# Optimization experiments

Hardware: AMD Instinct MI355X
Metric: run time of the kernel (lower is better)

## Reference

```python
import jax, jax.numpy as jnp
import numpy as np

IN_DIM = 1024
OUT_DIM = 1024
NHEAD = 16
K = 9  # template(1032) - dim(1024) + 1


def _slinear(vec, template, conv_w, conv_b, lin_b):
    # Conv2d over template produces the [out_dim, in_dim] weight matrix.
    w = jax.lax.conv_general_dilated(
        template, conv_w, window_strides=(1, 1), padding='VALID',
        dimension_numbers=('NCHW', 'OIHW', 'NCHW'))  # [1,1,out_dim,in_dim]
    w = w[0, 0] + conv_b  # broadcast conv bias (scalar per out-channel)
    return vec @ w.T + lin_b  # F.linear(vec, w) + bias


def setup_inputs() -> dict:
    key = jax.random.key(0)
    ks = jax.random.split(key, 13)
    S, B = 2048, 2
    d = {
        'query': jax.random.normal(ks[0], (S, B, IN_DIM), jnp.float32),
        'key': jax.random.normal(ks[1], (S, B, IN_DIM), jnp.float32),
        'value': jax.random.normal(ks[2], (S, B, IN_DIM), jnp.float32),
        'template': jax.random.normal(ks[3], (1, 1, 1032, 1032), jnp.float32),
    }
    for i, name in enumerate(['wq', 'wk', 'wv']):
        d[name + '_cw'] = jax.random.normal(ks[4 + 3 * i], (1, 1, K, K), jnp.float32) * 0.05
        d[name + '_cb'] = jax.random.normal(ks[5 + 3 * i], (1,), jnp.float32) * 0.05
        d[name + '_b'] = jax.random.normal(ks[6 + 3 * i], (OUT_DIM,), jnp.float32) * 0.05
    return d


def reference(query, key, value, template,
              wq_cw, wq_cb, wq_b, wk_cw, wk_cb, wk_b, wv_cw, wv_cb, wv_b):
    q = _slinear(query, template, wq_cw, wq_cb, wq_b)
    k = _slinear(key, template, wk_cw, wk_cb, wk_b)
    v = _slinear(value, template, wv_cw, wv_cb, wv_b)
    S, B = q.shape[0], q.shape[1]
    h_dim = OUT_DIM // NHEAD
    scale = h_dim ** 0.5
    qh = q.reshape(S, B, NHEAD, h_dim)
    kh = k.reshape(S, B, NHEAD, h_dim)
    vh = v.reshape(S, B, NHEAD, h_dim)
    # batch_first=False path: scores then softmax over last dim
    scores = jnp.einsum('ibhd,jbhd->bhij', qh, kh) / scale  # [B,H,S,S]
    attn = jax.nn.softmax(scores, axis=-1)
    out = jnp.einsum('bhij,jbhd->ibhd', attn, vh).reshape(S, B, OUT_DIM)
    return out
```

## Files before the change

### kernel.cpp

```cpp
#include <hip/hip_runtime.h>
#include <math.h>

#define TDIM   1032
#define DIM    1024
#define SLEN   2048
#define BATCH  2
#define NROWS  (SLEN*BATCH)
#define NHEAD  16
#define HD     64

typedef unsigned short u16;
typedef short short8 __attribute__((ext_vector_type(8)));
typedef short bf16x4 __attribute__((ext_vector_type(4)));
typedef float f32x4  __attribute__((ext_vector_type(4)));

#define CSCALE 0.18033688011112042f

__device__ inline unsigned fbits(float x) {
    union { float f; unsigned u; } v; v.f = x; return v.u;
}
__device__ inline float asfloat(unsigned u) {
    union { unsigned u; float f; } v; v.u = u; return v.f;
}
__device__ inline u16 f2bf_rne(float x) {
    unsigned u = fbits(x);
    unsigned r = u + 0x7fffu + ((u >> 16) & 1u);
    return (u16)(r >> 16);
}
__device__ inline float bf2f(u16 b) { return asfloat(((unsigned)b) << 16); }
__device__ inline void dma16(const u16* g, u16* l) {
    __builtin_amdgcn_global_load_lds(
        (const __attribute__((address_space(1))) void*)g,
        (__attribute__((address_space(3))) void*)l, 16, 0, 0);
}

__global__ __launch_bounds__(256) void conv_weight_kernel(
    const float* __restrict__ tmpl,
    const float* __restrict__ cw0, const float* __restrict__ cb0,
    const float* __restrict__ cw1, const float* __restrict__ cb1,
    const float* __restrict__ cw2, const float* __restrict__ cb2,
    u16* __restrict__ Wh, u16* __restrict__ Wl)
{
    int t = blockIdx.z;
    const float* cw = (t == 0) ? cw0 : ((t == 1) ? cw1 : cw2);
    const float* cb = (t == 0) ? cb0 : ((t == 1) ? cb1 : cb2);
    __shared__ float scw[81];
    if (threadIdx.x < 81) scw[threadIdx.x] = cw[threadIdx.x];
    __syncthreads();
    int i = blockIdx.x * 256 + threadIdx.x;
    int o = blockIdx.y;
    float acc = cb[0];
    #pragma unroll
    for (int dy = 0; dy < 9; ++dy) {
        const float* trow = tmpl + (size_t)(o + dy) * TDIM + i;
        #pragma unroll
        for (int dx = 0; dx < 9; ++dx)
            acc = fmaf(scw[dy * 9 + dx], trow[dx], acc);
    }
    size_t idx = (size_t)t * DIM * DIM + (size_t)o * DIM + i;
    u16 h = f2bf_rne(acc);
    Wh[idx] = h;
    Wl[idx] = f2bf_rne(acc - bf2f(h));
}

__global__ __launch_bounds__(256, 3) void qkv_mfma_gemm(
    const float* __restrict__ x0, const float* __restrict__ x1,
    const float* __restrict__ x2,
    const u16* __restrict__ Whg, const u16* __restrict__ Wlg,
    const float* __restrict__ b0, const float* __restrict__ b1,
    const float* __restrict__ b2,
    u16* __restrict__ Qh, u16* __restrict__ Ql,
    u16* __restrict__ Kh, u16* __restrict__ Kl,
    u16* __restrict__ Vb)
{
    int t = blockIdx.z;
    const float* X    = (t == 0) ? x0 : ((t == 1) ? x1 : x2);
    const u16* Bh_g   = Whg + (size_t)t * DIM * DIM;
    const u16* Bl_g   = Wlg + (size_t)t * DIM * DIM;
    const float* bias = (t == 0) ? b0 : ((t == 1) ? b1 : b2);

    __shared__ __align__(16) u16 lds[16384];
    u16* sAh = lds;
    u16* sAl = lds + 4096;
    u16* sBh = lds + 8192;
    u16* sBl = lds + 12288;

    int tid = threadIdx.x;
    int w = tid >> 6, lane = tid & 63;
    int c = lane & 15, quad = lane >> 4;
    int m0 = blockIdx.y * 128, n0 = blockIdx.x * 128;
    int mh = (w >> 1) * 64, nh = (w & 1) * 64;

    int arow = w * 32 + (lane & 31);
    int acol = (lane >> 5) * 16;
    const float* aptr = X + (size_t)(m0 + arow) * DIM + acol;

    int srow = lane >> 2, sgr = lane & 3;

    f32x4 acc[4][4];
    #pragma unroll
    for (int i = 0; i < 4; ++i)
        #pragma unroll
        for (int j = 0; j < 4; ++j)
            #pragma unroll
            for (int r = 0; r < 4; ++r) acc[i][j][r] = 0.0f;

    float bias_v[4];
    #pragma unroll
    for (int tn = 0; tn < 4; ++tn) bias_v[tn] = bias[n0 + nh + tn * 16 + c];

    float4 xa[4];
    #pragma unroll
    for (int i = 0; i < 2; ++i) {
        int rb = w * 32 + i * 16;
        const u16* gh = Bh_g + (size_t)(n0 + rb + srow) * DIM + sgr * 8;
        const u16* gl = Bl_g + (size_t)(n0 + rb + srow) * DIM + sgr * 8;
        dma16(gh, sBh + rb * 32);
        dma16(gl, sBl + rb * 32);
    }
    #pragma unroll
    for (int j = 0; j < 4; ++j) xa[j] = *(const float4*)(aptr + j * 4);

    for (int it = 0; it < 32; ++it) {
        #pragma unroll
        for (int g = 0; g < 2; ++g) {
            float v[8] = { xa[2*g].x, xa[2*g].y, xa[2*g].z, xa[2*g].w,
                           xa[2*g+1].x, xa[2*g+1].y, xa[2*g+1].z, xa[2*g+1].w };
            short8 hv, lv;
            #pragma unroll
            for (int e = 0; e < 8; ++e) {
                unsigned u = fbits(v[e]);
                hv[e] = (short)(u >> 16);
                float l = v[e] - asfloat(u & 0xffff0000u);
                lv[e] = (short)(fbits(l) >> 16);
            }
            *(short8*)(sAh + arow * 32 + acol + g * 8) = hv;
            *(short8*)(sAl + arow * 32 + acol + g * 8) = lv;
        }
        __syncthreads();

        short8 ah[4], al[4], bh[4], bl[4];
        #pragma unroll
        for (int tt = 0; tt < 4; ++tt) {
            int mi = (mh + tt * 16 + c) * 32 + quad * 8;
            ah[tt] = *(short8*)(sAh + mi);
            al[tt] = *(short8*)(sAl + mi);
            int ni = (nh + tt * 16 + c) * 32 + quad * 8;
            bh[tt] = *(short8*)(sBh + ni);
            bl[tt] = *(short8*)(sBl + ni);
        }
        __syncthreads();

        if (it < 31) {
            int kg = (it + 1) * 4;
            #pragma unroll
            for (int i = 0; i < 2; ++i) {
                int rb = w * 32 + i * 16;
                const u16* gh = Bh_g + (size_t)(n0 + rb + srow) * DIM + (kg + sgr) * 8;
                const u16* gl = Bl_g + (size_t)(n0 + rb + srow) * DIM + (kg + sgr) * 8;
                dma16(gh, sBh + rb * 32);
                dma16(gl, sBl + rb * 32);
            }
            #pragma unroll
            for (int j = 0; j < 4; ++j)
                xa[j] = *(const float4*)(aptr + (it + 1) * 32 + j * 4);
        }

        #pragma unroll
        for (int tm = 0; tm < 4; ++tm)
            #pragma unroll
            for (int tn = 0; tn < 4; ++tn) {
                acc[tm][tn] = __builtin_amdgcn_mfma_f32_16x16x32_bf16(
                    ah[tm], bh[tn], acc[tm][tn], 0, 0, 0);
                acc[tm][tn] = __builtin_amdgcn_mfma_f32_16x16x32_bf16(
                    ah[tm], bl[tn], acc[tm][tn], 0, 0, 0);
                acc[tm][tn] = __builtin_amdgcn_mfma_f32_16x16x32_bf16(
                    al[tm], bh[tn], acc[tm][tn], 0, 0, 0);
            }
    }

    if (t < 2) {
        u16* Yh = (t == 0) ? Qh : Kh;
        u16* Yl = (t == 0) ? Ql : Kl;
        float qs = (t == 0) ? CSCALE : 1.0f;
        #pragma unroll
        for (int tm = 0; tm < 4; ++tm)
            #pragma unroll
            for (int r = 0; r < 4; ++r) {
                int m = m0 + mh + tm * 16 + quad * 4 + r;
                #pragma unroll
                for (int tn = 0; tn < 4; ++tn) {
                    int n = n0 + nh + tn * 16 + c;
                    float o = (acc[tm][tn][r] + bias_v[tn]) * qs;
                    unsigned bo = fbits(o);
                    Yh[(size_t)m * DIM + n] = (u16)(bo >> 16);
                    float l = o - asfloat(bo & 0xffff0000u);
                    Yl[(size_t)m * DIM + n] = (u16)(fbits(l) >> 16);
                }
            }
    } else {
        #pragma unroll
        for (int tm = 0; tm < 4; ++tm)
            #pragma unroll
            for (int r = 0; r < 4; ++r) {
                int m = m0 + mh + tm * 16 + quad * 4 + r;
                #pragma unroll
                for (int tn = 0; tn < 4; ++tn) {
                    int n = n0 + nh + tn * 16 + c;
                    Vb[(size_t)m * DIM + n] =
                        (u16)(fbits(acc[tm][tn][r] + bias_v[tn]) >> 16);
                }
            }
    }
}

__global__ __launch_bounds__(256) void vt_kernel(
    const u16* __restrict__ Vb, u16* __restrict__ Vt)
{
    int b = blockIdx.z, h = blockIdx.y, s0 = blockIdx.x * 64;
    __shared__ __align__(16) u16 tile[64][80];
    int tid = threadIdx.x;
    int sl = tid >> 2, d0 = (tid & 3) * 16;
    const u16* src = Vb + (size_t)((s0 + sl) * BATCH + b) * DIM + h * HD + d0;
    short8 v0 = *(const short8*)src;
    short8 v1 = *(const short8*)(src + 8);
    #pragma unroll
    for (int j = 0; j < 8; ++j) {
        tile[d0 + j][sl] = (u16)v0[j];
        tile[d0 + 8 + j][sl] = (u16)v1[j];
    }
    __syncthreads();
    int d = tid >> 2, sc0 = (tid & 3) * 16;
    u16* dst = Vt + (size_t)((b * NHEAD + h) * HD + d) * SLEN + s0 + sc0;
    *(short8*)dst = *(const short8*)&tile[d][sc0];
    *(short8*)(dst + 8) = *(const short8*)&tile[d][sc0 + 8];
}

__global__ __launch_bounds__(256) void attn_mfma_kernel(
    const u16* __restrict__ Qh, const u16* __restrict__ Ql,
    const u16* __restrict__ Kh, const u16* __restrict__ Kl,
    const u16* __restrict__ Vt, float* __restrict__ out)
{
    int b = blockIdx.z, h = blockIdx.y;
    int q0 = blockIdx.x * 128;
    int tid = threadIdx.x;
    int w = tid >> 6, lane = tid & 63;
    int c = lane & 15, quad = lane >> 4;

    __shared__ __align__(16) u16 sbuf[2][3][4096];
    __shared__ __align__(16) u16 sP[4][2048];

    short8 qhf[2][2], qlf[2][2];
    #pragma unroll
    for (int u = 0; u < 2; ++u) {
        int s = q0 + w * 32 + u * 16 + c;
        size_t base = (size_t)(s * BATCH + b) * DIM + h * HD + quad * 8;
        qhf[u][0] = *(const short8*)(Qh + base);
        qhf[u][1] = *(const short8*)(Qh + base + 32);
        qlf[u][0] = *(const short8*)(Ql + base);
        qlf[u][1] = *(const short8*)(Ql + base + 32);
    }

    f32x4 acc[2][4];
    #pragma unroll
    for (int u = 0; u < 2; ++u)
        #pragma unroll
        for (int i = 0; i < 4; ++i)
            #pragma unroll
            for (int r = 0; r < 4; ++r) acc[u][i][r] = 0.0f;
    float m_run[2] = {-1e38f, -1e38f}, l_run[2] = {0.0f, 0.0f};

    int r3 = lane >> 3, c3 = lane & 7;
    int sw = c3 ^ r3;
    const size_t bhofs = (size_t)(b * NHEAD + h) * HD;

    #define ISSUE_DMA(n0v, bufv) do {                                          \
        _Pragma("unroll")                                                      \
        for (int j = 0; j < 2; ++j) {                                          \
            int i_ = 2 * w + j;                                                \
            int row_ = i_ * 8 + r3;                                            \
            size_t gk = (size_t)(((n0v) + row_) * BATCH + b) * DIM + h * HD + sw * 8; \
            dma16(Kh + gk, &sbuf[bufv][0][i_ * 512]);                          \
            dma16(Kl + gk, &sbuf[bufv][1][i_ * 512]);                          \
            size_t gv = (bhofs + row_) * SLEN + (n0v) + sw * 8;                \
            dma16(Vt + gv, &sbuf[bufv][2][i_ * 512]);                          \
        }                                                                      \
    } while (0)

    ISSUE_DMA(0, 0);

    for (int it = 0; it < 32; ++it) {
        int cur = it & 1;
        __syncthreads();
        if (it < 31) ISSUE_DMA((it + 1) * 64, cur ^ 1);

        const u16* bKh = sbuf[cur][0];
        const u16* bKl = sbuf[cur][1];
        const u16* bVt = sbuf[cur][2];

        f32x4 sc[2][4];
        #pragma unroll
        for (int ct = 0; ct < 4; ++ct) {
            int row = ct * 16 + c, rw = row & 7;
            int kb = row * 64;
            short8 kh0 = *(const short8*)(bKh + kb + ((quad ^ rw) * 8));
            short8 kh1 = *(const short8*)(bKh + kb + (((4 + quad) ^ rw) * 8));
            short8 kl0 = *(const short8*)(bKl + kb + ((quad ^ rw) * 8));
            short8 kl1 = *(const short8*)(bKl + kb + (((4 + quad) ^ rw) * 8));
            #pragma unroll
            for (int u = 0; u < 2; ++u) {
                f32x4 s = {0.0f, 0.0f, 0.0f, 0.0f};
                s = __builtin_amdgcn_mfma_f32_16x16x32_bf16(kh0, qhf[u][0], s, 0, 0, 0);
                s = __builtin_amdgcn_mfma_f32_16x16x32_bf16(kh1, qhf[u][1], s, 0, 0, 0);
                s = __builtin_amdgcn_mfma_f32_16x16x32_bf16(kh0, qlf[u][0], s, 0, 0, 0);
                s = __builtin_amdgcn_mfma_f32_16x16x32_bf16(kh1, qlf[u][1], s, 0, 0, 0);
                s = __builtin_amdgcn_mfma_f32_16x16x32_bf16(kl0, qhf[u][0], s, 0, 0, 0);
                s = __builtin_amdgcn_mfma_f32_16x16x32_bf16(kl1, qhf[u][1], s, 0, 0, 0);
                sc[u][ct] = s;
            }
        }

        u16* wp = sP[w];
        #pragma unroll
        for (int u = 0; u < 2; ++u) {
            float pm = sc[u][0][0];
            #pragma unroll
            for (int ct = 0; ct < 4; ++ct)
                #pragma unroll
                for (int r = 0; r < 4; ++r)
                    pm = fmaxf(pm, sc[u][ct][r]);
            pm = fmaxf(pm, __shfl_xor(pm, 16));
            pm = fmaxf(pm, __shfl_xor(pm, 32));
            float mnew = fmaxf(m_run[u], pm);
            float al = exp2f(m_run[u] - mnew);
            m_run[u] = mnew;
            float ps = 0.0f;
            int prow = (u * 16 + c) * 64;
            #pragma unroll
            for (int ct = 0; ct < 4; ++ct) {
                bf16x4 pk;
                #pragma unroll
                for (int r = 0; r < 4; ++r) {
                    float p = exp2f(sc[u][ct][r] - mnew);
                    ps += p;
                    pk[r] = (short)(fbits(p) >> 16);
                }
                int phys = (ct * 2 + (quad >> 1)) ^ (c & 7);
                *(bf16x4*)(wp + prow + phys * 8 + (quad & 1) * 4) = pk;
            }
            ps += __shfl_xor(ps, 16);
            ps += __shfl_xor(ps, 32);
            l_run[u] = l_run[u] * al + ps;

            float alr[4];
            #pragma unroll
            for (int r = 0; r < 4; ++r)
                alr[r] = __shfl(al, (lane & 48) | (quad * 4 + r));
            #pragma unroll
            for (int ctd = 0; ctd < 4; ++ctd)
                #pragma unroll
                for (int r = 0; r < 4; ++r) acc[u][ctd][r] *= alr[r];
        }

        short8 pf[2][2];
        #pragma unroll
        for (int u = 0; u < 2; ++u) {
            int prow = (u * 16 + c) * 64, rw = c & 7;
            pf[u][0] = *(const short8*)(wp + prow + ((quad ^ rw) * 8));
            pf[u][1] = *(const short8*)(wp + prow + (((4 + quad) ^ rw) * 8));
        }
        #pragma unroll
        for (int ctd = 0; ctd < 4; ++ctd) {
            int vrow = ctd * 16 + c, vrw = vrow & 7;
            int vb = vrow * 64;
            short8 v0 = *(const short8*)(bVt + vb + ((quad ^ vrw) * 8));
            short8 v1 = *(const short8*)(bVt + vb + (((4 + quad) ^ vrw) * 8));
            #pragma unroll
            for (int u = 0; u < 2; ++u) {
                acc[u][ctd] = __builtin_amdgcn_mfma_f32_16x16x32_bf16(
                    pf[u][0], v0, acc[u][ctd], 0, 0, 0);
                acc[u][ctd] = __builtin_amdgcn_mfma_f32_16x16x32_bf16(
                    pf[u][1], v1, acc[u][ctd], 0, 0, 0);
            }
        }
    }
    #undef ISSUE_DMA

    #pragma unroll
    for (int u = 0; u < 2; ++u) {
        float rl[4];
        #pragma unroll
        for (int r = 0; r < 4; ++r)
            rl[r] = 1.0f / __shfl(l_run[u], (lane & 48) | (quad * 4 + r));
        #pragma unroll
        for (int ctd = 0; ctd < 4; ++ctd)
            #pragma unroll
            for (int r = 0; r < 4; ++r) {
                int s = q0 + w * 32 + u * 16 + quad * 4 + r;
                out[(size_t)(s * BATCH + b) * DIM + h * HD + ctd * 16 + c] =
                    acc[u][ctd][r] * rl[r];
            }
    }
}

extern "C" void kernel_launch(void* const* d_in, const int* in_sizes, int n_in,
                              void* d_out, int out_size, void* d_ws, size_t ws_size,
                              hipStream_t stream)
{
    const float* query = (const float*)d_in[0];
    const float* key_  = (const float*)d_in[1];
    const float* value = (const float*)d_in[2];
    const float* tmpl  = (const float*)d_in[3];
    const float* wq_cw = (const float*)d_in[4];
    const float* wq_cb = (const float*)d_in[5];
    const float* wq_b  = (const float*)d_in[6];
    const float* wk_cw = (const float*)d_in[7];
    const float* wk_cb = (const float*)d_in[8];
    const float* wk_b  = (const float*)d_in[9];
    const float* wv_cw = (const float*)d_in[10];
    const float* wv_cb = (const float*)d_in[11];
    const float* wv_b  = (const float*)d_in[12];

    char* ws = (char*)d_ws;
    u16* Wh = (u16*)(ws);
    u16* Wl = (u16*)(ws + 6291456);
    u16* Qh = (u16*)(ws + 12582912);
    u16* Ql = (u16*)(ws + 20971520);
    u16* Kh = (u16*)(ws + 29360128);
    u16* Kl = (u16*)(ws + 37748736);
    u16* Vb = (u16*)(ws + 46137344);
    u16* Vt = (u16*)(ws + 54525952);
    float* out = (float*)d_out;

    conv_weight_kernel<<<dim3(DIM / 256, DIM, 3), 256, 0, stream>>>(
        tmpl, wq_cw, wq_cb, wk_cw, wk_cb, wv_cw, wv_cb, Wh, Wl);

    qkv_mfma_gemm<<<dim3(DIM / 128, NROWS / 128, 3), 256, 0, stream>>>(
        query, key_, value, Wh, Wl, wq_b, wk_b, wv_b, Qh, Ql, Kh, Kl, Vb);

    vt_kernel<<<dim3(SLEN / 64, NHEAD, BATCH), 256, 0, stream>>>(Vb, Vt);

    attn_mfma_kernel<<<dim3(SLEN / 128, NHEAD, BATCH), 256, 0, stream>>>(
        Qh, Ql, Kh, Kl, Vt, out);
}
```

Measured before the change: 339.2 us.

## Double-buffer QKV GEMM LDS tiles and skip low-part MFMAs for V

Converts the QKV projection GEMM to double-buffered LDS. The next K-slice's weight DMA and the A-tile conversion are issued before computing on the current buffer, which drops one barrier per iteration. For the V projection (t==2) it loads only the high bf16 parts and does a single MFMA per tile instead of three, since V is stored at bf16 precision. The change doubles LDS use and lowers launch-bounds occupancy from 3 to 2 blocks per CU, and V loses the compensated split-precision accuracy.

```diff
diff --git a/kernel.cpp b/kernel.cpp
--- a/kernel.cpp
+++ b/kernel.cpp
@@ -63,7 +63,7 @@
     Wl[idx] = f2bf_rne(acc - bf2f(h));
 }
 
-__global__ __launch_bounds__(256, 3) void qkv_mfma_gemm(
+__global__ __launch_bounds__(256, 2) void qkv_mfma_gemm(
     const float* __restrict__ x0, const float* __restrict__ x1,
     const float* __restrict__ x2,
     const u16* __restrict__ Whg, const u16* __restrict__ Wlg,
@@ -79,11 +79,8 @@
     const u16* Bl_g   = Wlg + (size_t)t * DIM * DIM;
     const float* bias = (t == 0) ? b0 : ((t == 1) ? b1 : b2);
 
-    __shared__ __align__(16) u16 lds[16384];
-    u16* sAh = lds;
-    u16* sAl = lds + 4096;
-    u16* sBh = lds + 8192;
-    u16* sBl = lds + 12288;
+    __shared__ __align__(16) u16 sAh[2][4096], sAl[2][4096];
+    __shared__ __align__(16) u16 sBh[2][4096], sBl[2][4096];
 
     int tid = threadIdx.x;
     int w = tid >> 6, lane = tid & 63;
@@ -109,75 +106,98 @@
     #pragma unroll
     for (int tn = 0; tn < 4; ++tn) bias_v[tn] = bias[n0 + nh + tn * 16 + c];
 
+    #define ISSUE_BDMA(itv, bufv) do {                                         \
+        int kg_ = (itv) * 4;                                                   \
+        _Pragma("unroll")                                                      \
+        for (int i_ = 0; i_ < 2; ++i_) {                                       \
+            int rb_ = w * 32 + i_ * 16;                                        \
+            const u16* gh_ = Bh_g + (size_t)(n0 + rb_ + srow) * DIM + (kg_ + sgr) * 8; \
+            dma16(gh_, sBh[bufv] + rb_ * 32);                                  \
+            if (t < 2) {                                                       \
+                const u16* gl_ = Bl_g + (size_t)(n0 + rb_ + srow) * DIM + (kg_ + sgr) * 8; \
+                dma16(gl_, sBl[bufv] + rb_ * 32);                              \
+            }                                                                  \
+        }                                                                      \
+    } while (0)
+
+    #define WRITE_A(bufv) do {                                                 \
+        _Pragma("unroll")                                                      \
+        for (int g_ = 0; g_ < 2; ++g_) {                                       \
+            float v_[8] = { xa[2*g_].x, xa[2*g_].y, xa[2*g_].z, xa[2*g_].w,    \
+                            xa[2*g_+1].x, xa[2*g_+1].y, xa[2*g_+1].z, xa[2*g_+1].w }; \
+            short8 hv_, lv_;                                                   \
+            _Pragma("unroll")                                                  \
+            for (int e_ = 0; e_ < 8; ++e_) {                                   \
+                unsigned u_ = fbits(v_[e_]);                                   \
+                hv_[e_] = (short)(u_ >> 16);                                   \
+                if (t < 2) {                                                   \
+                    float l_ = v_[e_] - asfloat(u_ & 0xffff0000u);             \
+                    lv_[e_] = (short)(fbits(l_) >> 16);                        \
+                }                                                              \
+            }                                                                  \
+            *(short8*)(sAh[bufv] + arow * 32 + acol + g_ * 8) = hv_;           \
+            if (t < 2)                                                         \
+                *(short8*)(sAl[bufv] + arow * 32 + acol + g_ * 8) = lv_;       \
+        }                                                                      \
+    } while (0)
+
     float4 xa[4];
-    #pragma unroll
-    for (int i = 0; i < 2; ++i) {
-        int rb = w * 32 + i * 16;
-        const u16* gh = Bh_g + (size_t)(n0 + rb + srow) * DIM + sgr * 8;
-        const u16* gl = Bl_g + (size_t)(n0 + rb + srow) * DIM + sgr * 8;
-        dma16(gh, sBh + rb * 32);
-        dma16(gl, sBl + rb * 32);
-    }
+    ISSUE_BDMA(0, 0);
     #pragma unroll
     for (int j = 0; j < 4; ++j) xa[j] = *(const float4*)(aptr + j * 4);
+    WRITE_A(0);
+    #pragma unroll
+    for (int j = 0; j < 4; ++j) xa[j] = *(const float4*)(aptr + 32 + j * 4);
+    __syncthreads();
 
     for (int it = 0; it < 32; ++it) {
-        #pragma unroll
-        for (int g = 0; g < 2; ++g) {
-            float v[8] = { xa[2*g].x, xa[2*g].y, xa[2*g].z, xa[2*g].w,
-                           xa[2*g+1].x, xa[2*g+1].y, xa[2*g+1].z, xa[2*g+1].w };
-            short8 hv, lv;
-            #pragma unroll
-            for (int e = 0; e < 8; ++e) {
-                unsigned u = fbits(v[e]);
-                hv[e] = (short)(u >> 16);
-                float l = v[e] - asfloat(u & 0xffff0000u);
-                lv[e] = (short)(fbits(l) >> 16);
-            }
-            *(short8*)(sAh + arow * 32 + acol + g * 8) = hv;
-            *(short8*)(sAl + arow * 32 + acol + g * 8) = lv;
+        int cur = it & 1;
+        if (it < 31) {
+            ISSUE_BDMA(it + 1, cur ^ 1);
+            WRITE_A(cur ^ 1);
+            if (it < 30) {
+                #pragma unroll
+                for (int j = 0; j < 4; ++j)
+                    xa[j] = *(const float4*)(aptr + (it + 2) * 32 + j * 4);
+            }
+        }
+
+        short8 ah[4], bh[4];
+        #pragma unroll
+        for (int tt = 0; tt < 4; ++tt) {
+            ah[tt] = *(short8*)(sAh[cur] + (mh + tt * 16 + c) * 32 + quad * 8);
+            bh[tt] = *(short8*)(sBh[cur] + (nh + tt * 16 + c) * 32 + quad * 8);
+        }
+        if (t < 2) {
+            short8 al[4], bl[4];
+            #pragma unroll
+            for (int tt = 0; tt < 4; ++tt) {
+                al[tt] = *(short8*)(sAl[cur] + (mh + tt * 16 + c) * 32 + quad * 8);
+                bl[tt] = *(short8*)(sBl[cur] + (nh + tt * 16 + c) * 32 + quad * 8);
+            }
+            #pragma unroll
+            for (int tm = 0; tm < 4; ++tm)
+                #pragma unroll
+                for (int tn = 0; tn < 4; ++tn) {
+                    acc[tm][tn] = __builtin_amdgcn_mfma_f32_16x16x32_bf16(
+                        ah[tm], bh[tn], acc[tm][tn], 0, 0, 0);
+                    acc[tm][tn] = __builtin_amdgcn_mfma_f32_16x16x32_bf16(
+                        ah[tm], bl[tn], acc[tm][tn], 0, 0, 0);
+                    acc[tm][tn] = __builtin_amdgcn_mfma_f32_16x16x32_bf16(
+                        al[tm], bh[tn], acc[tm][tn], 0, 0, 0);
+                }
+        } else {
+            #pragma unroll
+            for (int tm = 0; tm < 4; ++tm)
+                #pragma unroll
+                for (int tn = 0; tn < 4; ++tn)
+                    acc[tm][tn] = __builtin_amdgcn_mfma_f32_16x16x32_bf16(
+                        ah[tm], bh[tn], acc[tm][tn], 0, 0, 0);
         }
         __syncthreads();
-
-        short8 ah[4], al[4], bh[4], bl[4];
-        #pragma unroll
-        for (int tt = 0; tt < 4; ++tt) {
-            int mi = (mh + tt * 16 + c) * 32 + quad * 8;
-            ah[tt] = *(short8*)(sAh + mi);
-            al[tt] = *(short8*)(sAl + mi);
-            int ni = (nh + tt * 16 + c) * 32 + quad * 8;
-            bh[tt] = *(short8*)(sBh + ni);
-            bl[tt] = *(short8*)(sBl + ni);
-        }
-        __syncthreads();
-
-        if (it < 31) {
-            int kg = (it + 1) * 4;
-            #pragma unroll
-            for (int i = 0; i < 2; ++i) {
-                int rb = w * 32 + i * 16;
-                const u16* gh = Bh_g + (size_t)(n0 + rb + srow) * DIM + (kg + sgr) * 8;
-                const u16* gl = Bl_g + (size_t)(n0 + rb + srow) * DIM + (kg + sgr) * 8;
-                dma16(gh, sBh + rb * 32);
-                dma16(gl, sBl + rb * 32);
-            }
-            #pragma unroll
-            for (int j = 0; j < 4; ++j)
-                xa[j] = *(const float4*)(aptr + (it + 1) * 32 + j * 4);
-        }
-
-        #pragma unroll
-        for (int tm = 0; tm < 4; ++tm)
-            #pragma unroll
-            for (int tn = 0; tn < 4; ++tn) {
-                acc[tm][tn] = __builtin_amdgcn_mfma_f32_16x16x32_bf16(
-                    ah[tm], bh[tn], acc[tm][tn], 0, 0, 0);
-                acc[tm][tn] = __builtin_amdgcn_mfma_f32_16x16x32_bf16(
-                    ah[tm], bl[tn], acc[tm][tn], 0, 0, 0);
-                acc[tm][tn] = __builtin_amdgcn_mfma_f32_16x16x32_bf16(
-                    al[tm], bh[tn], acc[tm][tn], 0, 0, 0);
-            }
-    }
+    }
+    #undef ISSUE_BDMA
+    #undef WRITE_A
 
     if (t < 2) {
         u16* Yh = (t == 0) ? Qh : Kh;
```

Result: no change. 345.8 us (+2.0%).
